# Performance work log

Measured on AMD Instinct MI355X. Metric: run time of the kernel, lower is better.

The kernel has to match this reference:

```python
import jax, jax.numpy as jnp
import numpy as np

B = 65536
H = W = 28
K = 3
OUT_HW = H - K + 1  # 26, valid conv
FEAT = OUT_HW * OUT_HW  # 676
HID = 200
NCLS = 10


def setup_inputs() -> dict:
    key = jax.random.key(0)
    ks = jax.random.split(key, 6)
    x = jax.random.normal(ks[0], (B, H * W), dtype=jnp.float32)
    conv_w = jnp.ones((K, K), dtype=jnp.float32)  # Parameter(ones((3,3)))
    w1 = jax.random.normal(ks[1], (FEAT, HID), dtype=jnp.float32) * (1.0 / np.sqrt(FEAT))
    b1 = jnp.zeros((HID,), dtype=jnp.float32)
    w2 = jax.random.normal(ks[2], (HID, NCLS), dtype=jnp.float32) * (1.0 / np.sqrt(HID))
    b2 = jnp.zeros((NCLS,), dtype=jnp.float32)
    return {"x": x, "conv_w": conv_w, "w1": w1, "b1": b1, "w2": w2, "b2": b2}


def _forward(x, conv_w, w1, b1, w2, b2):
    img = x.reshape(-1, H, W)  # (B,28,28)
    # valid 3x3 single-channel cross-correlation (matches input[i:i+3,j:j+3]*w)
    lhs = img[:, None, :, :]          # (B,1,28,28)
    rhs = conv_w[None, None, :, :]    # (1,1,3,3)
    conv = jax.lax.conv_general_dilated(
        lhs, rhs, window_strides=(1, 1), padding="VALID",
        dimension_numbers=("NCHW", "OIHW", "NCHW"))  # (B,1,26,26)
    feat = conv.reshape(-1, FEAT)     # (B,676)
    hidden = jax.nn.relu(feat @ w1 + b1)  # (B,200)
    return hidden @ w2 + b2               # (B,10) logits


def reference(x, conv_w, w1, b1, w2, b2):
    return _forward(x, conv_w, w1, b1, w2, b2)
```

## Files before the change

### kernel.cpp

```cpp
#include <hip/hip_runtime.h>
#include <hip/hip_bf16.h>

#define BATCH   65536
#define HW      28
#define OHW     26
#define FEAT    676
#define HID     200
#define NCLS    10
#define MT2     64
#define GBLOCKS (BATCH / MT2)
#define KC1     25

typedef __attribute__((ext_vector_type(8))) __bf16 bf16x8;
typedef __attribute__((ext_vector_type(4))) float  f32x4;

#define KBAR() asm volatile("s_waitcnt lgkmcnt(0)\n\ts_barrier" ::: "memory")

__device__ __forceinline__ unsigned int pk2(float a, float b) {
  __hip_bfloat16 ha = __float2bfloat16(a), hb = __float2bfloat16(b);
  return (unsigned int)__builtin_bit_cast(unsigned short, ha)
       | ((unsigned int)__builtin_bit_cast(unsigned short, hb) << 16);
}

__device__ __forceinline__ uint4 pk8(float4 f0, float4 f1) {
  return make_uint4(pk2(f0.x, f0.y), pk2(f0.z, f0.w),
                    pk2(f1.x, f1.y), pk2(f1.z, f1.w));
}

__device__ __forceinline__ unsigned short* fslot(unsigned short* base, int m, int k) {
  const int kc = k >> 5;
  return base + ((kc * 64 + ((k >> 3) & 3) * 16 + (m ^ (kc & 7))) * 8) + (k & 7);
}

__global__ __launch_bounds__(256) void prep_w1e(const float* __restrict__ w1,
                                                const float* __restrict__ cwp,
                                                unsigned short* __restrict__ w1e) {
  int c = blockIdx.x * 256 + threadIdx.x;
  if (c >= KC1 * 13 * 64) return;
  int lane = c & 63, g = c >> 6;
  int kc = g / 13, nt = g - kc * 13;
  int ln = lane & 15, qd = lane >> 4;
  int n = nt * 16 + ln;
  float cw[9];
  #pragma unroll
  for (int t = 0; t < 9; ++t) cw[t] = cwp[t];
  float v[8];
  #pragma unroll
  for (int j = 0; j < 8; ++j) {
    int k = kc * 32 + qd * 8 + j;
    float s = 0.f;
    if (k < 784 && n < HID) {
      int ri = k / 28, ci = k - ri * 28;
      #pragma unroll
      for (int di = 0; di < 3; ++di) {
        int r = ri - di;
        if (r >= 0 && r < OHW) {
          #pragma unroll
          for (int dj = 0; dj < 3; ++dj) {
            int cc = ci - dj;
            if (cc >= 0 && cc < OHW) s += cw[di * 3 + dj] * w1[(r * OHW + cc) * HID + n];
          }
        }
      }
    }
    v[j] = s;
  }
  uint4 o = make_uint4(pk2(v[0], v[1]), pk2(v[2], v[3]),
                       pk2(v[4], v[5]), pk2(v[6], v[7]));
  *(uint4*)(w1e + (size_t)c * 8) = o;
}

__global__ __launch_bounds__(256) void prep_w2f(const float* __restrict__ w2,
                                                unsigned short* __restrict__ w2f) {
  int c = blockIdx.x * 256 + threadIdx.x;
  if (c >= 7 * 64) return;
  int lane = c & 63, kc = c >> 6;
  int col = lane & 15;
  float v[8];
  #pragma unroll
  for (int j = 0; j < 8; ++j) {
    int k = kc * 32 + (lane >> 4) * 8 + j;
    v[j] = (col < NCLS && k < HID) ? w2[k * NCLS + col] : 0.f;
  }
  uint4 o = make_uint4(pk2(v[0], v[1]), pk2(v[2], v[3]),
                       pk2(v[4], v[5]), pk2(v[6], v[7]));
  *(uint4*)(w2f + (size_t)c * 8) = o;
}

template<int NT0, int NT>
__device__ __forceinline__ void gemm1_body(
    const float* __restrict__ x, const unsigned short* __restrict__ w1e,
    const float* __restrict__ b1, unsigned short* aBuf ,
    unsigned short* hidA, int lane, int tid, int blk64) {
  const int ln = lane & 15, qd = lane >> 4;

  const int sc_qd = (tid >> 4) & 3;
  const float* xrow =
      x + ((size_t)blk64 + (tid >> 6) * 16 + (tid & 15)) * 784 + sc_qd * 8;

  f32x4 acc[4][NT];
  #pragma unroll
  for (int mi = 0; mi < 4; ++mi)
    #pragma unroll
    for (int t = 0; t < NT; ++t) acc[mi][t] = (f32x4){0.f, 0.f, 0.f, 0.f};

  {
    float4 p0 = *(const float4*)(xrow);
    float4 p1 = *(const float4*)(xrow + 4);
    *(uint4*)(aBuf + tid * 8) = pk8(p0, p1);
  }
  float4 a1l0 = *(const float4*)(xrow + 32), a1l1 = *(const float4*)(xrow + 36);
  float4 a2l0 = *(const float4*)(xrow + 64), a2l1 = *(const float4*)(xrow + 68);
  bf16x8 bCur[NT];
  #pragma unroll
  for (int t = 0; t < NT; ++t)
    bCur[t] = *(const bf16x8*)(w1e + ((size_t)((NT0 + t) * 64 + lane)) * 8);
  __syncthreads();

  #pragma unroll
  for (int kc = 0; kc < KC1; ++kc) {
    if (kc + 1 < KC1)
      *(uint4*)(aBuf + ((kc + 1) & 1) * 2048 + tid * 8) = pk8(a1l0, a1l1);
    a1l0 = a2l0; a1l1 = a2l1;

    bf16x8 bNx[NT];
    if (kc + 1 < KC1) {
      #pragma unroll
      for (int t = 0; t < NT; ++t)
        bNx[t] = *(const bf16x8*)(w1e +
                   ((size_t)((kc + 1) * 13 + NT0 + t) * 64 + lane) * 8);
    }
    if (kc + 3 < KC1) {
      if (kc + 3 == KC1 - 1 && sc_qd >= 2) {
        a2l0 = (float4){0.f, 0.f, 0.f, 0.f};
        a2l1 = (float4){0.f, 0.f, 0.f, 0.f};
      } else {
        a2l0 = *(const float4*)(xrow + (kc + 3) * 32);
        a2l1 = *(const float4*)(xrow + (kc + 3) * 32 + 4);
      }
    }

    const unsigned short* ab = aBuf + (kc & 1) * 2048;
    bf16x8 a[4];
    #pragma unroll
    for (int mi = 0; mi < 4; ++mi)
      a[mi] = *(const bf16x8*)(ab + mi * 512 + lane * 8);
    #pragma unroll
    for (int t = 0; t < NT; ++t)
      #pragma unroll
      for (int mi = 0; mi < 4; ++mi)
        acc[mi][t] = __builtin_amdgcn_mfma_f32_16x16x32_bf16(a[mi], bCur[t],
                                                             acc[mi][t], 0, 0, 0);
    if (kc + 1 < KC1) {
      #pragma unroll
      for (int t = 0; t < NT; ++t) bCur[t] = bNx[t];
    }
    KBAR();
  }

  #pragma unroll
  for (int t = 0; t < NT; ++t) {
    const int n = (NT0 + t) * 16 + ln;
    if (n < HID) {
      const float bias = b1[n];
      const int kc2 = n >> 5, qd2 = (n >> 3) & 3, j2 = n & 7, c2 = kc2 & 7;
      #pragma unroll
      for (int mi = 0; mi < 4; ++mi)
        #pragma unroll
        for (int rr = 0; rr < 4; ++rr) {
          const int m = qd * 4 + rr;
          float h = fmaxf(acc[mi][t][rr] + bias, 0.f);
          __hip_bfloat16 hb = __float2bfloat16(h);
          hidA[mi * 3584 + (kc2 * 64 + qd2 * 16 + (m ^ c2)) * 8 + j2] =
              __builtin_bit_cast(unsigned short, hb);
        }
    }
  }
}

__global__ __launch_bounds__(256, 3) void fused8(
    const float* __restrict__ x, const unsigned short* __restrict__ w1e,
    const unsigned short* __restrict__ w2f, const float* __restrict__ b1,
    const float* __restrict__ b2, float* __restrict__ out) {
  __shared__ __align__(16) unsigned short aBuf[2 * 2048];
  __shared__ __align__(16) unsigned short hidA[4 * 7 * 64 * 8];
  const int tid  = threadIdx.x;
  const int wave = tid >> 6;
  const int lane = tid & 63;
  const int blk64 = blockIdx.x * MT2;

  for (int i = tid; i < 768; i += 256) {
    int mi = i / 192, r = i - mi * 192, m = r / 12, d = r - m * 12;
    *(unsigned int*)fslot(hidA + mi * 3584, m, 200 + 2 * d) = 0u;
  }

  switch (wave) {
    case 0:  gemm1_body<0, 4>(x, w1e, b1, aBuf, hidA, lane, tid, blk64); break;
    case 1:  gemm1_body<4, 3>(x, w1e, b1, aBuf, hidA, lane, tid, blk64); break;
    case 2:  gemm1_body<7, 3>(x, w1e, b1, aBuf, hidA, lane, tid, blk64); break;
    default: gemm1_body<10, 3>(x, w1e, b1, aBuf, hidA, lane, tid, blk64); break;
  }
  __syncthreads();

  const int ln = lane & 15, qd = lane >> 4;
  f32x4 acc2 = (f32x4){0.f, 0.f, 0.f, 0.f};
  #pragma unroll
  for (int kc = 0; kc < 7; ++kc) {
    bf16x8 a = *(const bf16x8*)&hidA[wave * 3584 + (kc * 64 + (lane ^ (kc & 7))) * 8];
    bf16x8 b = *(const bf16x8*)(w2f + ((size_t)kc * 64 + lane) * 8);
    acc2 = __builtin_amdgcn_mfma_f32_16x16x32_bf16(a, b, acc2, 0, 0, 0);
  }
  if (ln < NCLS) {
    const float bb = b2[ln];
    #pragma unroll
    for (int rr = 0; rr < 4; ++rr) {
      out[((size_t)(blockIdx.x * 4 + wave) * 16 + qd * 4 + rr) * NCLS + ln] = acc2[rr] + bb;
    }
  }
}

extern "C" void kernel_launch(void* const* d_in, const int* in_sizes, int n_in,
                              void* d_out, int out_size, void* d_ws, size_t ws_size,
                              hipStream_t stream) {
  const float* x  = (const float*)d_in[0];
  const float* cw = (const float*)d_in[1];
  const float* w1 = (const float*)d_in[2];
  const float* b1 = (const float*)d_in[3];
  const float* w2 = (const float*)d_in[4];
  const float* b2 = (const float*)d_in[5];
  float* out = (float*)d_out;

  unsigned short* w1e = (unsigned short*)d_ws;
  unsigned short* w2f = (unsigned short*)((char*)d_ws + 335872);

  hipLaunchKernelGGL(prep_w1e, dim3((KC1 * 13 * 64 + 255) / 256), dim3(256), 0, stream,
                     w1, cw, w1e);
  hipLaunchKernelGGL(prep_w2f, dim3(2), dim3(256), 0, stream, w2, w2f);
  hipLaunchKernelGGL(fused8, dim3(GBLOCKS), dim3(256), 0, stream,
                     x, w1e, w2f, b1, b2, out);
}
```

Baseline: 328.0 us.

## Stage whole 32-row input tile in swizzled LDS, drop per-chunk barriers

Instead of double-buffering 32-column K chunks of x with a barrier per chunk, each block now loads all 784 columns of 32 rows into one XOR-swizzled LDS tile up front, then runs the 25-step MFMA loop with no barriers. The batch tile shrinks from 64 to 32 rows, which doubles the grid, and the LDS tile is reused for the hidden activations. This removes per-iteration synchronisation and makes global loads coalesced row reads. The cost is less overlap between loading and compute, fewer MFMAs per B-fragment load, and only half the waves doing the second GEMM.

After: 345.4 us. 1.05x slower.

```diff
diff --git a/kernel.cpp b/kernel.cpp
--- a/kernel.cpp
+++ b/kernel.cpp
@@ -4,27 +4,20 @@
 #define BATCH   65536
 #define HW      28
 #define OHW     26
-#define FEAT    676
 #define HID     200
 #define NCLS    10
-#define MT2     64
+#define MT2     32
 #define GBLOCKS (BATCH / MT2)
 #define KC1     25
+#define RSH     832
 
 typedef __attribute__((ext_vector_type(8))) __bf16 bf16x8;
 typedef __attribute__((ext_vector_type(4))) float  f32x4;
-
-#define KBAR() asm volatile("s_waitcnt lgkmcnt(0)\n\ts_barrier" ::: "memory")
 
 __device__ __forceinline__ unsigned int pk2(float a, float b) {
   __hip_bfloat16 ha = __float2bfloat16(a), hb = __float2bfloat16(b);
   return (unsigned int)__builtin_bit_cast(unsigned short, ha)
        | ((unsigned int)__builtin_bit_cast(unsigned short, hb) << 16);
-}
-
-__device__ __forceinline__ uint4 pk8(float4 f0, float4 f1) {
-  return make_uint4(pk2(f0.x, f0.y), pk2(f0.z, f0.w),
-                    pk2(f1.x, f1.y), pk2(f1.z, f1.w));
 }
 
 __device__ __forceinline__ unsigned short* fslot(unsigned short* base, int m, int k) {
@@ -88,41 +81,16 @@
 }
 
 template<int NT0, int NT>
-__device__ __forceinline__ void gemm1_body(
-    const float* __restrict__ x, const unsigned short* __restrict__ w1e,
-    const float* __restrict__ b1, unsigned short* aBuf ,
-    unsigned short* hidA, int lane, int tid, int blk64) {
+__device__ __forceinline__ void gemm1_compute(
+    const unsigned short* __restrict__ w1e, const unsigned short* sh,
+    int lane, f32x4 (&acc)[2][4]) {
   const int ln = lane & 15, qd = lane >> 4;
-
-  const int sc_qd = (tid >> 4) & 3;
-  const float* xrow =
-      x + ((size_t)blk64 + (tid >> 6) * 16 + (tid & 15)) * 784 + sc_qd * 8;
-
-  f32x4 acc[4][NT];
-  #pragma unroll
-  for (int mi = 0; mi < 4; ++mi)
-    #pragma unroll
-    for (int t = 0; t < NT; ++t) acc[mi][t] = (f32x4){0.f, 0.f, 0.f, 0.f};
-
-  {
-    float4 p0 = *(const float4*)(xrow);
-    float4 p1 = *(const float4*)(xrow + 4);
-    *(uint4*)(aBuf + tid * 8) = pk8(p0, p1);
-  }
-  float4 a1l0 = *(const float4*)(xrow + 32), a1l1 = *(const float4*)(xrow + 36);
-  float4 a2l0 = *(const float4*)(xrow + 64), a2l1 = *(const float4*)(xrow + 68);
   bf16x8 bCur[NT];
   #pragma unroll
   for (int t = 0; t < NT; ++t)
     bCur[t] = *(const bf16x8*)(w1e + ((size_t)((NT0 + t) * 64 + lane)) * 8);
-  __syncthreads();
-
-  #pragma unroll
+  const int sw = (ln & 7) << 3;
   for (int kc = 0; kc < KC1; ++kc) {
-    if (kc + 1 < KC1)
-      *(uint4*)(aBuf + ((kc + 1) & 1) * 2048 + tid * 8) = pk8(a1l0, a1l1);
-    a1l0 = a2l0; a1l1 = a2l1;
-
     bf16x8 bNx[NT];
     if (kc + 1 < KC1) {
       #pragma unroll
@@ -130,34 +98,28 @@
         bNx[t] = *(const bf16x8*)(w1e +
                    ((size_t)((kc + 1) * 13 + NT0 + t) * 64 + lane) * 8);
     }
-    if (kc + 3 < KC1) {
-      if (kc + 3 == KC1 - 1 && sc_qd >= 2) {
-        a2l0 = (float4){0.f, 0.f, 0.f, 0.f};
-        a2l1 = (float4){0.f, 0.f, 0.f, 0.f};
-      } else {
-        a2l0 = *(const float4*)(xrow + (kc + 3) * 32);
-        a2l1 = *(const float4*)(xrow + (kc + 3) * 32 + 4);
-      }
-    }
-
-    const unsigned short* ab = aBuf + (kc & 1) * 2048;
-    bf16x8 a[4];
-    #pragma unroll
-    for (int mi = 0; mi < 4; ++mi)
-      a[mi] = *(const bf16x8*)(ab + mi * 512 + lane * 8);
+    bf16x8 a[2];
+    #pragma unroll
+    for (int mi = 0; mi < 2; ++mi)
+      a[mi] = *(const bf16x8*)&sh[(((mi * 16 + ln) * RSH) + kc * 32 + qd * 8) ^ sw];
     #pragma unroll
     for (int t = 0; t < NT; ++t)
       #pragma unroll
-      for (int mi = 0; mi < 4; ++mi)
+      for (int mi = 0; mi < 2; ++mi)
         acc[mi][t] = __builtin_amdgcn_mfma_f32_16x16x32_bf16(a[mi], bCur[t],
                                                              acc[mi][t], 0, 0, 0);
     if (kc + 1 < KC1) {
       #pragma unroll
       for (int t = 0; t < NT; ++t) bCur[t] = bNx[t];
     }
-    KBAR();
-  }
-
+  }
+}
+
+template<int NT0, int NT>
+__device__ __forceinline__ void gemm1_epilogue(
+    const float* __restrict__ b1, unsigned short* hidA, int lane,
+    f32x4 (&acc)[2][4]) {
+  const int ln = lane & 15, qd = lane >> 4;
   #pragma unroll
   for (int t = 0; t < NT; ++t) {
     const int n = (NT0 + t) * 16 + ln;
@@ -165,7 +127,7 @@
       const float bias = b1[n];
       const int kc2 = n >> 5, qd2 = (n >> 3) & 3, j2 = n & 7, c2 = kc2 & 7;
       #pragma unroll
-      for (int mi = 0; mi < 4; ++mi)
+      for (int mi = 0; mi < 2; ++mi)
         #pragma unroll
         for (int rr = 0; rr < 4; ++rr) {
           const int m = qd * 4 + rr;
@@ -178,43 +140,80 @@
   }
 }
 
-__global__ __launch_bounds__(256, 3) void fused8(
+__global__ __launch_bounds__(256, 3) void fused9(
     const float* __restrict__ x, const unsigned short* __restrict__ w1e,
     const unsigned short* __restrict__ w2f, const float* __restrict__ b1,
     const float* __restrict__ b2, float* __restrict__ out) {
-  __shared__ __align__(16) unsigned short aBuf[2 * 2048];
-  __shared__ __align__(16) unsigned short hidA[4 * 7 * 64 * 8];
+  __shared__ __align__(16) unsigned short sh[MT2 * RSH];
   const int tid  = threadIdx.x;
   const int wave = tid >> 6;
   const int lane = tid & 63;
-  const int blk64 = blockIdx.x * MT2;
-
-  for (int i = tid; i < 768; i += 256) {
+  const int blk32 = blockIdx.x * MT2;
+
+  #pragma unroll
+  for (int r8 = 0; r8 < 8; ++r8) {
+    const int row = wave * 8 + r8;
+    const float* xr = x + (size_t)(blk32 + row) * 784;
+    const int base = row * RSH;
+    const int swz = (row & 7) << 3;
+    #pragma unroll
+    for (int i = 0; i < 3; ++i) {
+      const int e = i * 256 + lane * 4;
+      const float4 f = *(const float4*)(xr + e);
+      *(uint2*)&sh[(base + e) ^ swz] = make_uint2(pk2(f.x, f.y), pk2(f.z, f.w));
+    }
+    if (lane < 4) {
+      const int e = 768 + lane * 4;
+      const float4 f = *(const float4*)(xr + e);
+      *(uint2*)&sh[(base + e) ^ swz] = make_uint2(pk2(f.x, f.y), pk2(f.z, f.w));
+    } else if (lane < 16) {
+      const int e = 768 + lane * 4;
+      *(uint2*)&sh[(base + e) ^ swz] = make_uint2(0u, 0u);
+    }
+  }
+  __syncthreads();
+
+  f32x4 acc[2][4];
+  #pragma unroll
+  for (int mi = 0; mi < 2; ++mi)
+    #pragma unroll
+    for (int t = 0; t < 4; ++t) acc[mi][t] = (f32x4){0.f, 0.f, 0.f, 0.f};
+  switch (wave) {
+    case 0:  gemm1_compute<0, 4>(w1e, sh, lane, acc); break;
+    case 1:  gemm1_compute<4, 3>(w1e, sh, lane, acc); break;
+    case 2:  gemm1_compute<7, 3>(w1e, sh, lane, acc); break;
+    default: gemm1_compute<10, 3>(w1e, sh, lane, acc); break;
+  }
+  __syncthreads();
+
+  for (int i = tid; i < 384; i += 256) {
     int mi = i / 192, r = i - mi * 192, m = r / 12, d = r - m * 12;
-    *(unsigned int*)fslot(hidA + mi * 3584, m, 200 + 2 * d) = 0u;
-  }
-
+    *(unsigned int*)fslot(sh + mi * 3584, m, 200 + 2 * d) = 0u;
+  }
   switch (wave) {
-    case 0:  gemm1_body<0, 4>(x, w1e, b1, aBuf, hidA, lane, tid, blk64); break;
-    case 1:  gemm1_body<4, 3>(x, w1e, b1, aBuf, hidA, lane, tid, blk64); break;
-    case 2:  gemm1_body<7, 3>(x, w1e, b1, aBuf, hidA, lane, tid, blk64); break;
-    default: gemm1_body<10, 3>(x, w1e, b1, aBuf, hidA, lane, tid, blk64); break;
+    case 0:  gemm1_epilogue<0, 4>(b1, sh, lane, acc); break;
+    case 1:  gemm1_epilogue<4, 3>(b1, sh, lane, acc); break;
+    case 2:  gemm1_epilogue<7, 3>(b1, sh, lane, acc); break;
+    default: gemm1_epilogue<10, 3>(b1, sh, lane, acc); break;
   }
   __syncthreads();
 
-  const int ln = lane & 15, qd = lane >> 4;
-  f32x4 acc2 = (f32x4){0.f, 0.f, 0.f, 0.f};
-  #pragma unroll
-  for (int kc = 0; kc < 7; ++kc) {
-    bf16x8 a = *(const bf16x8*)&hidA[wave * 3584 + (kc * 64 + (lane ^ (kc & 7))) * 8];
-    bf16x8 b = *(const bf16x8*)(w2f + ((size_t)kc * 64 + lane) * 8);
-    acc2 = __builtin_amdgcn_mfma_f32_16x16x32_bf16(a, b, acc2, 0, 0, 0);
-  }
-  if (ln < NCLS) {
-    const float bb = b2[ln];
-    #pragma unroll
-    for (int rr = 0; rr < 4; ++rr) {
-      out[((size_t)(blockIdx.x * 4 + wave) * 16 + qd * 4 + rr) * NCLS + ln] = acc2[rr] + bb;
+  if (wave < 2) {
+    const int ln = lane & 15, qd = lane >> 4;
+    f32x4 acc2 = (f32x4){0.f, 0.f, 0.f, 0.f};
+    #pragma unroll
+    for (int kc = 0; kc < 7; ++kc) {
+      bf16x8 a = *(const bf16x8*)&sh[wave * 3584 + (kc * 64 + (lane ^ (kc & 7))) * 8];
+      bf16x8 b = *(const bf16x8*)(w2f + ((size_t)kc * 64 + lane) * 8);
+      acc2 = __builtin_amdgcn_mfma_f32_16x16x32_bf16(a, b, acc2, 0, 0, 0);
+    }
+    if (ln < NCLS) {
+      const float bb = b2[ln];
+      #pragma unroll
+      for (int rr = 0; rr < 4; ++rr) {
+        out[((size_t)(blockIdx.x * 2 + wave) * 16 + qd * 4 + rr) * NCLS + ln] =
+            acc2[rr] + bb;
+      }
     }
   }
 }
@@ -236,6 +235,6 @@
   hipLaunchKernelGGL(prep_w1e, dim3((KC1 * 13 * 64 + 255) / 256), dim3(256), 0, stream,
                      w1, cw, w1e);
   hipLaunchKernelGGL(prep_w2f, dim3(2), dim3(256), 0, stream, w2, w2f);
-  hipLaunchKernelGGL(fused8, dim3(GBLOCKS), dim3(256), 0, stream,
+  hipLaunchKernelGGL(fused9, dim3(GBLOCKS), dim3(256), 0, stream,
                      x, w1e, w2f, b1, b2, out);
 }
```
